# Kernel tuning notes

Hardware: AMD Instinct MI355X
Metric: run time of the kernel (lower is better)

Reference implementation:

```python
import jax, jax.numpy as jnp
import numpy as np

HEADS = 8

def setup_inputs() -> dict:
    key = jax.random.key(0)
    k1, k2, k3 = jax.random.split(key, 3)
    B, C, L = 8, 512, 4096
    dim_head = 64
    hidden = HEADS * dim_head  # 512
    x = jax.random.normal(k1, (B, C, L), dtype=jnp.float32)
    # Conv1d(dim, hidden*3, 1, bias=False) -> weight [hidden*3, dim]
    w_qkv = jax.random.normal(k2, (hidden * 3, C), dtype=jnp.float32) * 0.02
    # Conv1d(hidden, dim, 1) -> weight [dim, hidden], bias [dim]
    w_out = jax.random.normal(k3, (C, hidden), dtype=jnp.float32) * 0.02
    b_out = jnp.zeros((C,), dtype=jnp.float32)
    return {"x": x, "w_qkv": w_qkv, "w_out": w_out, "b_out": b_out}

def reference(x, w_qkv, w_out, b_out):
    B, C, L = x.shape
    # 1x1 Conv1d == channel matmul
    qkv = jnp.einsum('oc,bcl->bol', w_qkv, x)            # [B, 3*H*dh, L]
    qkv = qkv.reshape(B, 3, HEADS, -1, L)                # qkv outermost, then heads, then c
    q, k, v = qkv[:, 0], qkv[:, 1], qkv[:, 2]            # each [B, H, dh, L]
    k = jax.nn.softmax(k, axis=-1)                       # softmax over sequence
    context = jnp.einsum('bhdn,bhen->bhde', k, v)        # [B, H, dh, dh]
    out = jnp.einsum('bhde,bhdn->bhen', context, q)      # [B, H, dh, L]
    out = out.reshape(B, -1, L)                          # [B, H*dh, L]
    return jnp.einsum('oc,bcl->bol', w_out, out) + b_out[None, :, None]
```

## Files before the change

### kernel.cpp

```cpp
#include <hip/hip_runtime.h>
#include <hip/hip_bf16.h>


typedef __bf16 bf16x8 __attribute__((ext_vector_type(8)));
typedef __bf16 bf16x4 __attribute__((ext_vector_type(4)));
typedef float  f32x4  __attribute__((ext_vector_type(4)));

#define B_  8
#define L_  4096
#define C_  512

#define GLD_LDS16(g, l)                                             \
    __builtin_amdgcn_global_load_lds(                               \
        (const __attribute__((address_space(1))) void*)(g),         \
        (__attribute__((address_space(3))) void*)(l), 16, 0, 0)

__global__ __launch_bounds__(256) void prep(const float* __restrict__ wkv_f,
                                            __hip_bfloat16* __restrict__ wkv_b,
                                            __hip_bfloat16* __restrict__ wqT,
                                            float* __restrict__ ctx) {
    int blk = blockIdx.x;
    if (blk < 2048) {
        int i = blk * 256 + threadIdx.x;
        wkv_b[i] = __float2bfloat16(wkv_f[512 * 512 + i]);
    } else if (blk < 2048 + 256) {
        int tb = blk - 2048;
        int r0 = (tb >> 4) * 32, c0 = (tb & 15) * 32;
        __shared__ float tile[32][33];
        int tx = threadIdx.x & 31, ty = threadIdx.x >> 5;
        for (int r = 0; r < 32; r += 8)
            tile[ty + r][tx] = wkv_f[(size_t)(r0 + ty + r) * 512 + c0 + tx];
        __syncthreads();
        for (int r = 0; r < 32; r += 8)
            wqT[(size_t)(c0 + ty + r) * 512 + r0 + tx] = __float2bfloat16(tile[tx][ty + r]);
    } else {
        int i = (blk - 2304) * 256 + threadIdx.x;
        ctx[i] = 0.f;
    }
}

__global__ __launch_bounds__(256) void transpose_cvt(const float* __restrict__ x,
                                                     __hip_bfloat16* __restrict__ xt) {
    __shared__ float tile[64 * 132];
    int b = blockIdx.z;
    int l0 = blockIdx.x * 128, c0 = blockIdx.y * 64;
    int t = threadIdx.x;
    const float* xp = x + ((size_t)b * C_ + c0) * L_ + l0;
#pragma unroll
    for (int p = 0; p < 8; p++) {
        int i = p * 8 + (t >> 5);
        int j = (t & 31) * 4;
        float4 vv = *(const float4*)(xp + (size_t)i * L_ + j);
        *(float4*)&tile[i * 132 + j] = vv;
    }
    __syncthreads();
    unsigned short* xo = (unsigned short*)xt + ((size_t)b * L_ + l0) * C_ + c0;
#pragma unroll
    for (int qq = 0; qq < 8; qq++) {
        int l = qq * 16 + (t >> 4);
        int cg = (t & 15) * 4;
        bf16x4 ov;
#pragma unroll
        for (int k = 0; k < 4; k++) ov[k] = (__bf16)tile[(cg + k) * 132 + l];
        *(bf16x4*)(xo + (size_t)l * C_ + cg) = ov;
    }
}

template <int MODE>
__global__ __launch_bounds__(256) void gemm_bt(
    const __hip_bfloat16* __restrict__ A, const __hip_bfloat16* __restrict__ Bt,
    size_t strideA, size_t strideB, int M, int N, int K,
    __hip_bfloat16* __restrict__ kb, __hip_bfloat16* __restrict__ vb,
    __hip_bfloat16* __restrict__ obf,
    float* __restrict__ outb, const float* __restrict__ bias) {
    __shared__ alignas(16) unsigned short As[128 * 32];
    __shared__ alignas(16) unsigned short Bs[128 * 32];

    int b = blockIdx.z;
    int m0 = blockIdx.y * 128, n0 = blockIdx.x * 128;
    const __hip_bfloat16* Ab = A + strideA * (size_t)b;
    const __hip_bfloat16* Bb = Bt + strideB * (size_t)b;

    int t = threadIdx.x;
    int lane = t & 63, wv = t >> 6;
    int l16 = lane & 15, q4 = lane >> 4;
    int wr = (wv >> 1) * 64, wc = (wv & 1) * 64;

    int srow = lane >> 2;
    int skg  = lane & 3;
    int kc   = ((skg ^ (srow & 3)) * 8);

    const __hip_bfloat16* gA0 = Ab + (size_t)(m0 + wv * 32 + srow) * K + kc;
    const __hip_bfloat16* gA1 = gA0 + (size_t)16 * K;
    const __hip_bfloat16* gB0 = Bb + (size_t)(n0 + wv * 32 + srow) * K + kc;
    const __hip_bfloat16* gB1 = gB0 + (size_t)16 * K;
    unsigned short* lA0 = &As[(wv * 32) * 32];
    unsigned short* lA1 = &As[(wv * 32 + 16) * 32];
    unsigned short* lB0 = &Bs[(wv * 32) * 32];
    unsigned short* lB1 = &Bs[(wv * 32 + 16) * 32];

    int fsw = (q4 ^ (l16 & 3)) * 8;

    f32x4 acc[4][4] = {};

    for (int k0 = 0; k0 < K; k0 += 32) {
        __syncthreads();
        GLD_LDS16(gA0 + k0, lA0);
        GLD_LDS16(gA1 + k0, lA1);
        GLD_LDS16(gB0 + k0, lB0);
        GLD_LDS16(gB1 + k0, lB1);
        __syncthreads();

        bf16x8 af[4], bfr[4];
#pragma unroll
        for (int i = 0; i < 4; i++) {
            af[i]  = *(const bf16x8*)&As[(wr + i * 16 + l16) * 32 + fsw];
            bfr[i] = *(const bf16x8*)&Bs[(wc + i * 16 + l16) * 32 + fsw];
        }
#pragma unroll
        for (int i = 0; i < 4; i++)
#pragma unroll
            for (int j = 0; j < 4; j++)
                acc[i][j] = __builtin_amdgcn_mfma_f32_16x16x32_bf16(af[i], bfr[j], acc[i][j], 0, 0, 0);
    }

#pragma unroll
    for (int i = 0; i < 4; i++)
#pragma unroll
        for (int j = 0; j < 4; j++)
#pragma unroll
            for (int r = 0; r < 4; r++) {
                int row = m0 + wr + i * 16 + q4 * 4 + r;
                int col = n0 + wc + j * 16 + l16;
                float val = acc[i][j][r];
                if (MODE == 1) {
                    int part = row >> 9, od = row & 511;
                    size_t idx = ((size_t)b * 512 + od) * (size_t)N + col;
                    __hip_bfloat16 cv = __float2bfloat16(val);
                    if (part == 0) kb[idx] = cv;
                    else           vb[idx] = cv;
                } else if (MODE == 3) {
                    obf[((size_t)b * 512 + row) * (size_t)N + col] = __float2bfloat16(val);
                } else {
                    outb[((size_t)b * 512 + row) * (size_t)N + col] = val + bias[row];
                }
            }
}

__global__ __launch_bounds__(256) void softmax_k(const __hip_bfloat16* __restrict__ kin,
                                                 __hip_bfloat16* __restrict__ ks) {
    int row = blockIdx.x;
    const unsigned short* kp = (const unsigned short*)kin + (size_t)row * L_;
    __shared__ float buf[L_];
    __shared__ float red[8];
    int t = threadIdx.x, lane = t & 63, wv = t >> 6;
    float m = -1e30f;
    for (int i0 = t * 8; i0 < L_; i0 += 256 * 8) {
        bf16x8 kv = *(const bf16x8*)(kp + i0);
#pragma unroll
        for (int j = 0; j < 8; j++) {
            float x = (float)kv[j];
            buf[i0 + j] = x;
            m = fmaxf(m, x);
        }
    }
    for (int o = 32; o; o >>= 1) m = fmaxf(m, __shfl_xor(m, o, 64));
    if (lane == 0) red[wv] = m;
    __syncthreads();
    m = fmaxf(fmaxf(red[0], red[1]), fmaxf(red[2], red[3]));
    float s = 0.f;
    for (int i = t; i < L_; i += 256) { float e = __expf(buf[i] - m); buf[i] = e; s += e; }
    for (int o = 32; o; o >>= 1) s += __shfl_xor(s, o, 64);
    if (lane == 0) red[4 + wv] = s;
    __syncthreads();
    s = red[4] + red[5] + red[6] + red[7];
    float inv = 1.0f / s;
    unsigned short* op = (unsigned short*)ks + (size_t)row * L_;
    for (int i0 = t * 8; i0 < L_; i0 += 256 * 8) {
        bf16x8 ov;
#pragma unroll
        for (int j = 0; j < 8; j++) ov[j] = (__bf16)(buf[i0 + j] * inv);
        *(bf16x8*)(op + i0) = ov;
    }
}

__global__ __launch_bounds__(256) void ctx_kernel(const __hip_bfloat16* __restrict__ ks,
                                                  const __hip_bfloat16* __restrict__ v,
                                                  float* __restrict__ ctx) {
    int kc = blockIdx.x, h = blockIdx.y, b = blockIdx.z;
    int t = threadIdx.x, lane = t & 63, wv = t >> 6;
    int l16 = lane & 15, q4 = lane >> 4;
    const __hip_bfloat16* ka = ks + ((size_t)b * 512 + h * 64) * L_;
    const __hip_bfloat16* va = v + ((size_t)b * 512 + h * 64) * L_;
    f32x4 acc[4][4] = {};
    int nbase = kc * 512 + wv * 128;
#pragma unroll
    for (int s = 0; s < 4; s++) {
        int n = nbase + s * 32 + q4 * 8;
        bf16x8 af[4], bfr[4];
#pragma unroll
        for (int i = 0; i < 4; i++) {
            af[i]  = *(const bf16x8*)(ka + (size_t)(i * 16 + l16) * L_ + n);
            bfr[i] = *(const bf16x8*)(va + (size_t)(i * 16 + l16) * L_ + n);
        }
#pragma unroll
        for (int i = 0; i < 4; i++)
#pragma unroll
            for (int j = 0; j < 4; j++)
                acc[i][j] = __builtin_amdgcn_mfma_f32_16x16x32_bf16(af[i], bfr[j], acc[i][j], 0, 0, 0);
    }
    __shared__ float cbuf[4096];
    for (int w = 0; w < 4; w++) {
        if (wv == w) {
#pragma unroll
            for (int i = 0; i < 4; i++)
#pragma unroll
                for (int j = 0; j < 4; j++)
#pragma unroll
                    for (int r = 0; r < 4; r++) {
                        int mm = i * 16 + q4 * 4 + r, nn = j * 16 + l16;
                        float pv = acc[i][j][r];
                        if (w == 0) cbuf[mm * 64 + nn] = pv;
                        else        cbuf[mm * 64 + nn] += pv;
                    }
        }
        __syncthreads();
    }
    float* cg = ctx + ((size_t)b * 8 + h) * 4096;
    for (int i = t; i < 4096; i += 256) atomicAdd(&cg[i], cbuf[i]);
}

__global__ __launch_bounds__(256) void w2_kernel(const float* __restrict__ wout,
                                                 const float* __restrict__ ctx,
                                                 __hip_bfloat16* __restrict__ w2) {
    int ob = blockIdx.x, h = blockIdx.y, b = blockIdx.z;
    __shared__ float cT[64 * 65];
    __shared__ float wT[64 * 65];
    int t = threadIdx.x;
    const float* cg = ctx + ((size_t)b * 8 + h) * 4096;
    for (int i = t; i < 4096; i += 256) {
        int d = i >> 6, e = i & 63;
        cT[e * 65 + d] = cg[i];
        wT[e * 65 + d] = wout[(size_t)(ob * 64 + d) * 512 + h * 64 + e];
    }
    __syncthreads();
    int ol = t >> 2;
    int db = (t & 3) * 16;
    for (int dd = 0; dd < 16; dd++) {
        int d = db + dd;
        float s = 0.f;
#pragma unroll
        for (int e = 0; e < 64; e++) s += wT[e * 65 + ol] * cT[e * 65 + d];
        w2[((size_t)b * 512 + ob * 64 + ol) * 512 + h * 64 + d] = __float2bfloat16(s);
    }
}

extern "C" void kernel_launch(void* const* d_in, const int* in_sizes, int n_in,
                              void* d_out, int out_size, void* d_ws, size_t ws_size,
                              hipStream_t stream) {
    const float* x     = (const float*)d_in[0];
    const float* w_qkv = (const float*)d_in[1];
    const float* w_out = (const float*)d_in[2];
    const float* b_out = (const float*)d_in[3];
    float* out = (float*)d_out;
    char* ws = (char*)d_ws;

    const size_t QKV = (size_t)B_ * 512 * L_;
    size_t off_xt  = 0;
    size_t off_wkv = off_xt + (size_t)B_ * L_ * C_ * 2;
    size_t off_wqT = off_wkv + (size_t)1024 * 512 * 2;
    size_t off_k   = off_wqT + (size_t)512 * 512 * 2;
    size_t off_ks  = off_k + QKV * 2;
    size_t off_v   = off_ks + QKV * 2;
    size_t off_ctx = off_v + QKV * 2;
    size_t off_w2  = off_ctx + (size_t)B_ * 8 * 64 * 64 * 4;
    size_t off_w3  = off_w2 + (size_t)B_ * 512 * 512 * 2;

    __hip_bfloat16* xt   = (__hip_bfloat16*)(ws + off_xt);
    __hip_bfloat16* wkvb = (__hip_bfloat16*)(ws + off_wkv);
    __hip_bfloat16* wqT  = (__hip_bfloat16*)(ws + off_wqT);
    __hip_bfloat16* kb   = (__hip_bfloat16*)(ws + off_k);
    __hip_bfloat16* ksb  = (__hip_bfloat16*)(ws + off_ks);
    __hip_bfloat16* vb   = (__hip_bfloat16*)(ws + off_v);
    float*          ctx  = (float*)(ws + off_ctx);
    __hip_bfloat16* w2   = (__hip_bfloat16*)(ws + off_w2);
    __hip_bfloat16* W3   = (__hip_bfloat16*)(ws + off_w3);

    prep<<<3328, 256, 0, stream>>>(w_qkv, wkvb, wqT, ctx);
    transpose_cvt<<<dim3(L_ / 128, C_ / 64, B_), 256, 0, stream>>>(x, xt);

    gemm_bt<1><<<dim3(L_ / 128, 1024 / 128, B_), 256, 0, stream>>>(
        wkvb, xt, 0, (size_t)L_ * C_, 1024, L_, 512, kb, vb, nullptr, nullptr, nullptr);

    softmax_k<<<B_ * 512, 256, 0, stream>>>(kb, ksb);
    ctx_kernel<<<dim3(8, 8, B_), 256, 0, stream>>>(ksb, vb, ctx);
    w2_kernel<<<dim3(8, 8, B_), 256, 0, stream>>>(w_out, ctx, w2);

    gemm_bt<3><<<dim3(512 / 128, 512 / 128, B_), 256, 0, stream>>>(
        w2, wqT, (size_t)512 * 512, 0, 512, 512, 512, nullptr, nullptr, W3, nullptr, nullptr);

    gemm_bt<2><<<dim3(L_ / 128, 512 / 128, B_), 256, 0, stream>>>(
        W3, xt, (size_t)512 * 512, (size_t)L_ * C_, 512, L_, 512, nullptr, nullptr, nullptr, out, b_out);
}
```

Measured before the change: 281.3 us.

## Fuse softmax normalization into ctx kernel, merge prep kernels, widen GEMM K-tile

Replaces the softmax kernel that wrote a normalized bf16 K copy with a row-statistics kernel that writes only the per-row max and inverse sum. The ctx kernel now applies exp and scaling on the fly while loading K, which removes one full write and read of the K tensor. The transpose/convert kernel is also merged into the weight-prep kernel to save a launch. The GEMM K-tile is doubled from 32 to 64 with a new swizzle, halving the number of barrier pairs per tile at the cost of twice the shared memory.

```diff
diff --git a/kernel.cpp b/kernel.cpp
--- a/kernel.cpp
+++ b/kernel.cpp
@@ -15,54 +15,52 @@
         (const __attribute__((address_space(1))) void*)(g),         \
         (__attribute__((address_space(3))) void*)(l), 16, 0, 0)
 
-__global__ __launch_bounds__(256) void prep(const float* __restrict__ wkv_f,
-                                            __hip_bfloat16* __restrict__ wkv_b,
-                                            __hip_bfloat16* __restrict__ wqT,
-                                            float* __restrict__ ctx) {
+__global__ __launch_bounds__(256) void prep_all(const float* __restrict__ x,
+                                                __hip_bfloat16* __restrict__ xt,
+                                                const float* __restrict__ wqkv_f,
+                                                __hip_bfloat16* __restrict__ wkv_b,
+                                                __hip_bfloat16* __restrict__ wqT,
+                                                float* __restrict__ ctx) {
+    __shared__ float tile[64 * 132];
     int blk = blockIdx.x;
+    int t = threadIdx.x;
     if (blk < 2048) {
-        int i = blk * 256 + threadIdx.x;
-        wkv_b[i] = __float2bfloat16(wkv_f[512 * 512 + i]);
-    } else if (blk < 2048 + 256) {
-        int tb = blk - 2048;
+        int b = blk >> 8, rem = blk & 255;
+        int l0 = (rem & 31) * 128, c0 = (rem >> 5) * 64;
+        const float* xp = x + ((size_t)b * C_ + c0) * L_ + l0;
+#pragma unroll
+        for (int p = 0; p < 8; p++) {
+            int i = p * 8 + (t >> 5);
+            int j = (t & 31) * 4;
+            float4 vv = *(const float4*)(xp + (size_t)i * L_ + j);
+            *(float4*)&tile[i * 132 + j] = vv;
+        }
+        __syncthreads();
+        unsigned short* xo = (unsigned short*)xt + ((size_t)b * L_ + l0) * C_ + c0;
+#pragma unroll
+        for (int qq = 0; qq < 8; qq++) {
+            int l = qq * 16 + (t >> 4);
+            int cg = (t & 15) * 4;
+            bf16x4 ov;
+#pragma unroll
+            for (int k = 0; k < 4; k++) ov[k] = (__bf16)tile[(cg + k) * 132 + l];
+            *(bf16x4*)(xo + (size_t)l * C_ + cg) = ov;
+        }
+    } else if (blk < 4096) {
+        int i = (blk - 2048) * 256 + t;
+        wkv_b[i] = __float2bfloat16(wqkv_f[512 * 512 + i]);
+    } else if (blk < 4352) {
+        int tb = blk - 4096;
         int r0 = (tb >> 4) * 32, c0 = (tb & 15) * 32;
-        __shared__ float tile[32][33];
-        int tx = threadIdx.x & 31, ty = threadIdx.x >> 5;
+        int tx = t & 31, ty = t >> 5;
         for (int r = 0; r < 32; r += 8)
-            tile[ty + r][tx] = wkv_f[(size_t)(r0 + ty + r) * 512 + c0 + tx];
+            tile[(ty + r) * 33 + tx] = wqkv_f[(size_t)(r0 + ty + r) * 512 + c0 + tx];
         __syncthreads();
         for (int r = 0; r < 32; r += 8)
-            wqT[(size_t)(c0 + ty + r) * 512 + r0 + tx] = __float2bfloat16(tile[tx][ty + r]);
+            wqT[(size_t)(c0 + ty + r) * 512 + r0 + tx] = __float2bfloat16(tile[tx * 33 + ty + r]);
     } else {
-        int i = (blk - 2304) * 256 + threadIdx.x;
+        int i = (blk - 4352) * 256 + t;
         ctx[i] = 0.f;
-    }
-}
-
-__global__ __launch_bounds__(256) void transpose_cvt(const float* __restrict__ x,
-                                                     __hip_bfloat16* __restrict__ xt) {
-    __shared__ float tile[64 * 132];
-    int b = blockIdx.z;
-    int l0 = blockIdx.x * 128, c0 = blockIdx.y * 64;
-    int t = threadIdx.x;
-    const float* xp = x + ((size_t)b * C_ + c0) * L_ + l0;
-#pragma unroll
-    for (int p = 0; p < 8; p++) {
-        int i = p * 8 + (t >> 5);
-        int j = (t & 31) * 4;
-        float4 vv = *(const float4*)(xp + (size_t)i * L_ + j);
-        *(float4*)&tile[i * 132 + j] = vv;
-    }
-    __syncthreads();
-    unsigned short* xo = (unsigned short*)xt + ((size_t)b * L_ + l0) * C_ + c0;
-#pragma unroll
-    for (int qq = 0; qq < 8; qq++) {
-        int l = qq * 16 + (t >> 4);
-        int cg = (t & 15) * 4;
-        bf16x4 ov;
-#pragma unroll
-        for (int k = 0; k < 4; k++) ov[k] = (__bf16)tile[(cg + k) * 132 + l];
-        *(bf16x4*)(xo + (size_t)l * C_ + cg) = ov;
     }
 }
 
@@ -73,8 +71,8 @@
     __hip_bfloat16* __restrict__ kb, __hip_bfloat16* __restrict__ vb,
     __hip_bfloat16* __restrict__ obf,
     float* __restrict__ outb, const float* __restrict__ bias) {
-    __shared__ alignas(16) unsigned short As[128 * 32];
-    __shared__ alignas(16) unsigned short Bs[128 * 32];
+    __shared__ alignas(16) unsigned short As[128 * 64];
+    __shared__ alignas(16) unsigned short Bs[128 * 64];
 
     int b = blockIdx.z;
     int m0 = blockIdx.y * 128, n0 = blockIdx.x * 128;
@@ -86,36 +84,53 @@
     int l16 = lane & 15, q4 = lane >> 4;
     int wr = (wv >> 1) * 64, wc = (wv & 1) * 64;
 
-    int srow = lane >> 2;
-    int skg  = lane & 3;
-    int kc   = ((skg ^ (srow & 3)) * 8);
-
-    const __hip_bfloat16* gA0 = Ab + (size_t)(m0 + wv * 32 + srow) * K + kc;
-    const __hip_bfloat16* gA1 = gA0 + (size_t)16 * K;
-    const __hip_bfloat16* gB0 = Bb + (size_t)(n0 + wv * 32 + srow) * K + kc;
-    const __hip_bfloat16* gB1 = gB0 + (size_t)16 * K;
-    unsigned short* lA0 = &As[(wv * 32) * 32];
-    unsigned short* lA1 = &As[(wv * 32 + 16) * 32];
-    unsigned short* lB0 = &Bs[(wv * 32) * 32];
-    unsigned short* lB1 = &Bs[(wv * 32 + 16) * 32];
-
-    int fsw = (q4 ^ (l16 & 3)) * 8;
+    int srow = lane >> 3;
+    int swz  = ((lane & 7) ^ srow) * 8;
+
+    const __hip_bfloat16* gA[4];
+    const __hip_bfloat16* gB[4];
+    unsigned short* lA[4];
+    unsigned short* lB[4];
+#pragma unroll
+    for (int c = 0; c < 4; c++) {
+        int r = wv * 32 + c * 8;
+        gA[c] = Ab + (size_t)(m0 + r + srow) * K + swz;
+        gB[c] = Bb + (size_t)(n0 + r + srow) * K + swz;
+        lA[c] = &As[r * 64];
+        lB[c] = &Bs[r * 64];
+    }
+
+    int gsel0 = ((q4) ^ (l16 & 7)) * 8;
+    int gsel1 = ((4 + q4) ^ (l16 & 7)) * 8;
+    int rA = (wr + l16) * 64;
+    int rB = (wc + l16) * 64;
 
     f32x4 acc[4][4] = {};
 
-    for (int k0 = 0; k0 < K; k0 += 32) {
-        __syncthreads();
-        GLD_LDS16(gA0 + k0, lA0);
-        GLD_LDS16(gA1 + k0, lA1);
-        GLD_LDS16(gB0 + k0, lB0);
-        GLD_LDS16(gB1 + k0, lB1);
+    for (int k0 = 0; k0 < K; k0 += 64) {
+        __syncthreads();
+#pragma unroll
+        for (int c = 0; c < 4; c++) {
+            GLD_LDS16(gA[c] + k0, lA[c]);
+            GLD_LDS16(gB[c] + k0, lB[c]);
+        }
         __syncthreads();
 
         bf16x8 af[4], bfr[4];
 #pragma unroll
         for (int i = 0; i < 4; i++) {
-            af[i]  = *(const bf16x8*)&As[(wr + i * 16 + l16) * 32 + fsw];
-            bfr[i] = *(const bf16x8*)&Bs[(wc + i * 16 + l16) * 32 + fsw];
+            af[i]  = *(const bf16x8*)&As[rA + i * 1024 + gsel0];
+            bfr[i] = *(const bf16x8*)&Bs[rB + i * 1024 + gsel0];
+        }
+#pragma unroll
+        for (int i = 0; i < 4; i++)
+#pragma unroll
+            for (int j = 0; j < 4; j++)
+                acc[i][j] = __builtin_amdgcn_mfma_f32_16x16x32_bf16(af[i], bfr[j], acc[i][j], 0, 0, 0);
+#pragma unroll
+        for (int i = 0; i < 4; i++) {
+            af[i]  = *(const bf16x8*)&As[rA + i * 1024 + gsel1];
+            bfr[i] = *(const bf16x8*)&Bs[rB + i * 1024 + gsel1];
         }
 #pragma unroll
         for (int i = 0; i < 4; i++)
@@ -147,8 +162,9 @@
             }
 }
 
-__global__ __launch_bounds__(256) void softmax_k(const __hip_bfloat16* __restrict__ kin,
-                                                 __hip_bfloat16* __restrict__ ks) {
+__global__ __launch_bounds__(256) void rowstat(const __hip_bfloat16* __restrict__ kin,
+                                               float* __restrict__ mrow,
+                                               float* __restrict__ isrow) {
     int row = blockIdx.x;
     const unsigned short* kp = (const unsigned short*)kin + (size_t)row * L_;
     __shared__ float buf[L_];
@@ -159,9 +175,9 @@
         bf16x8 kv = *(const bf16x8*)(kp + i0);
 #pragma unroll
         for (int j = 0; j < 8; j++) {
-            float x = (float)kv[j];
-            buf[i0 + j] = x;
-            m = fmaxf(m, x);
+            float xx = (float)kv[j];
+            buf[i0 + j] = xx;
+            m = fmaxf(m, xx);
         }
     }
     for (int o = 32; o; o >>= 1) m = fmaxf(m, __shfl_xor(m, o, 64));
@@ -169,29 +185,34 @@
     __syncthreads();
     m = fmaxf(fmaxf(red[0], red[1]), fmaxf(red[2], red[3]));
     float s = 0.f;
-    for (int i = t; i < L_; i += 256) { float e = __expf(buf[i] - m); buf[i] = e; s += e; }
+    for (int i = t; i < L_; i += 256) s += __expf(buf[i] - m);
     for (int o = 32; o; o >>= 1) s += __shfl_xor(s, o, 64);
     if (lane == 0) red[4 + wv] = s;
     __syncthreads();
-    s = red[4] + red[5] + red[6] + red[7];
-    float inv = 1.0f / s;
-    unsigned short* op = (unsigned short*)ks + (size_t)row * L_;
-    for (int i0 = t * 8; i0 < L_; i0 += 256 * 8) {
-        bf16x8 ov;
-#pragma unroll
-        for (int j = 0; j < 8; j++) ov[j] = (__bf16)(buf[i0 + j] * inv);
-        *(bf16x8*)(op + i0) = ov;
-    }
-}
-
-__global__ __launch_bounds__(256) void ctx_kernel(const __hip_bfloat16* __restrict__ ks,
+    if (t == 0) {
+        s = red[4] + red[5] + red[6] + red[7];
+        mrow[row] = m;
+        isrow[row] = 1.0f / s;
+    }
+}
+
+__global__ __launch_bounds__(256) void ctx_kernel(const __hip_bfloat16* __restrict__ kraw,
+                                                  const float* __restrict__ mrow,
+                                                  const float* __restrict__ isrow,
                                                   const __hip_bfloat16* __restrict__ v,
                                                   float* __restrict__ ctx) {
     int kc = blockIdx.x, h = blockIdx.y, b = blockIdx.z;
     int t = threadIdx.x, lane = t & 63, wv = t >> 6;
     int l16 = lane & 15, q4 = lane >> 4;
-    const __hip_bfloat16* ka = ks + ((size_t)b * 512 + h * 64) * L_;
+    const __hip_bfloat16* ka = kraw + ((size_t)b * 512 + h * 64) * L_;
     const __hip_bfloat16* va = v + ((size_t)b * 512 + h * 64) * L_;
+    int rbase = b * 512 + h * 64;
+    float mr[4], ir[4];
+#pragma unroll
+    for (int i = 0; i < 4; i++) {
+        mr[i] = mrow[rbase + i * 16 + l16];
+        ir[i] = isrow[rbase + i * 16 + l16];
+    }
     f32x4 acc[4][4] = {};
     int nbase = kc * 512 + wv * 128;
 #pragma unroll
@@ -200,7 +221,10 @@
         bf16x8 af[4], bfr[4];
 #pragma unroll
         for (int i = 0; i < 4; i++) {
-            af[i]  = *(const bf16x8*)(ka + (size_t)(i * 16 + l16) * L_ + n);
+            bf16x8 kv = *(const bf16x8*)(ka + (size_t)(i * 16 + l16) * L_ + n);
+#pragma unroll
+            for (int e = 0; e < 8; e++)
+                af[i][e] = (__bf16)(__expf((float)kv[e] - mr[i]) * ir[i]);
             bfr[i] = *(const bf16x8*)(va + (size_t)(i * 16 + l16) * L_ + n);
         }
 #pragma unroll
@@ -270,9 +294,10 @@
     size_t off_wkv = off_xt + (size_t)B_ * L_ * C_ * 2;
     size_t off_wqT = off_wkv + (size_t)1024 * 512 * 2;
     size_t off_k   = off_wqT + (size_t)512 * 512 * 2;
-    size_t off_ks  = off_k + QKV * 2;
-    size_t off_v   = off_ks + QKV * 2;
-    size_t off_ctx = off_v + QKV * 2;
+    size_t off_v   = off_k + QKV * 2;
+    size_t off_ms  = off_v + QKV * 2;
+    size_t off_is  = off_ms + 4096 * 4;
+    size_t off_ctx = off_is + 4096 * 4;
     size_t off_w2  = off_ctx + (size_t)B_ * 8 * 64 * 64 * 4;
     size_t off_w3  = off_w2 + (size_t)B_ * 512 * 512 * 2;
 
@@ -280,20 +305,20 @@
     __hip_bfloat16* wkvb = (__hip_bfloat16*)(ws + off_wkv);
     __hip_bfloat16* wqT  = (__hip_bfloat16*)(ws + off_wqT);
     __hip_bfloat16* kb   = (__hip_bfloat16*)(ws + off_k);
-    __hip_bfloat16* ksb  = (__hip_bfloat16*)(ws + off_ks);
     __hip_bfloat16* vb   = (__hip_bfloat16*)(ws + off_v);
+    float*          ms   = (float*)(ws + off_ms);
+    float*          isv  = (float*)(ws + off_is);
     float*          ctx  = (float*)(ws + off_ctx);
     __hip_bfloat16* w2   = (__hip_bfloat16*)(ws + off_w2);
     __hip_bfloat16* W3   = (__hip_bfloat16*)(ws + off_w3);
 
-    prep<<<3328, 256, 0, stream>>>(w_qkv, wkvb, wqT, ctx);
-    transpose_cvt<<<dim3(L_ / 128, C_ / 64, B_), 256, 0, stream>>>(x, xt);
+    prep_all<<<5376, 256, 0, stream>>>(x, xt, w_qkv, wkvb, wqT, ctx);
 
     gemm_bt<1><<<dim3(L_ / 128, 1024 / 128, B_), 256, 0, stream>>>(
         wkvb, xt, 0, (size_t)L_ * C_, 1024, L_, 512, kb, vb, nullptr, nullptr, nullptr);
 
-    softmax_k<<<B_ * 512, 256, 0, stream>>>(kb, ksb);
-    ctx_kernel<<<dim3(8, 8, B_), 256, 0, stream>>>(ksb, vb, ctx);
+    rowstat<<<B_ * 512, 256, 0, stream>>>(kb, ms, isv);
+    ctx_kernel<<<dim3(8, 8, B_), 256, 0, stream>>>(kb, ms, isv, vb, ctx);
     w2_kernel<<<dim3(8, 8, B_), 256, 0, stream>>>(w_out, ctx, w2);
 
     gemm_bt<3><<<dim3(512 / 128, 512 / 128, B_), 256, 0, stream>>>(
```

Measured after the change: 261.1 us. -7.2%, faster.
